# Kernel tuning notes

Measured on AMD Instinct MI355X. Metric: run time of the kernel, lower is better.

Reference implementation:

```python
import jax, jax.numpy as jnp
import numpy as np

B, S, D_IN, D_OUT, DEPTH = 4, 2048, 2048, 2048, 11
N_NODES = 2 ** (DEPTH + 1) - 1  # 4095


def setup_inputs() -> dict:
    key = jax.random.key(0)
    k1, k2, k3 = jax.random.split(key, 3)
    x = jax.random.normal(k1, (B, S, D_IN), dtype=jnp.float32)
    # scale weights like Linear init (~1/sqrt(fan_in)) to keep logits sane
    w_in = jax.random.normal(k2, (N_NODES, D_IN), dtype=jnp.float32) * (1.0 / np.sqrt(D_IN))
    w_out = jax.random.normal(k3, (D_OUT, N_NODES), dtype=jnp.float32) * (1.0 / np.sqrt(N_NODES))
    return {"x": x, "w_in": w_in, "w_out": w_out}


def reference(x, w_in, w_out):
    # x: [B,S,D_in]; w_in: [n_nodes, D_in]; w_out: [D_out, n_nodes]
    b, s, _ = x.shape
    cur = jnp.zeros((b, s), dtype=jnp.int32)
    nodes, logits = [], []
    for _ in range(DEPTH + 1):  # fixed, small depth loop (12 iters)
        nodes.append(cur)
        coeffs = w_in[cur]                       # [B,S,D_in] data-dependent gather
        score = jnp.einsum('bsd,bsd->bs', x, coeffs)  # per-token dot product
        logits.append(score)
        cur = cur * 2 + (score >= 0).astype(jnp.int32) + 1
    all_nodes = jnp.stack(nodes, axis=-1)        # [B,S,depth+1]
    all_logits = jnp.stack(logits, axis=-1)      # [B,S,depth+1]
    sel = w_out.T[all_nodes]                     # [B,S,depth+1,D_out]
    mlp1 = jax.nn.gelu(all_logits, approximate=False)  # torch nn.GELU default = exact erf
    return jnp.einsum('bsl,bslw->bsw', mlp1, sel)      # [B,S,D_out]
```

## Files before the change

kernel.cpp:

```cpp
#include <hip/hip_runtime.h>


#define D_IN    2048
#define D_OUT   2048
#define DEPTHP1 12
#define N_NODES 4095
#define N_TOK   8192
#define N_LEAF  2048

typedef float f4 __attribute__((ext_vector_type(4)));

__global__ __launch_bounds__(256) void transpose_wout64(
    const float* __restrict__ in, float* __restrict__ out) {
    __shared__ float tile[64][65];
    const int n0 = blockIdx.x * 64;
    const int j0 = blockIdx.y * 64;
    const int tx = threadIdx.x;
    const int ty = threadIdx.y;
    const int n = n0 + tx;
#pragma unroll
    for (int k = 0; k < 16; k++) {
        const int r = ty * 16 + k;
        if (n < N_NODES) tile[r][tx] = in[(size_t)(j0 + r) * N_NODES + n];
    }
    __syncthreads();
#pragma unroll
    for (int k = 0; k < 16; k++) {
        const int r = ty * 16 + k;
        const int nn = n0 + r;
        if (nn < N_NODES) out[(size_t)nn * D_OUT + (j0 + tx)] = tile[tx][r];
    }
}

__global__ __launch_bounds__(256) void phaseA(
    const float* __restrict__ x,
    const float* __restrict__ w_in,
    float* __restrict__ g_all,
    int* __restrict__ leaf,
    int* __restrict__ hist) {
    extern __shared__ float xs[];
    const int wave  = threadIdx.x >> 6;
    const int lane  = threadIdx.x & 63;
    const int token = blockIdx.x * 4 + wave;

    float4* xw = (float4*)(xs) + wave * (D_IN / 4);
    const float4* xrow = (const float4*)(x + (size_t)token * D_IN);
#pragma unroll
    for (int c = 0; c < 8; c++) xw[lane + 64 * c] = xrow[lane + 64 * c];

    int cur = 0;
#pragma unroll
    for (int l = 0; l < DEPTHP1; l++) {
        const float4* wrow = (const float4*)(w_in + (size_t)cur * D_IN);
        float p0 = 0.f, p1 = 0.f, p2 = 0.f, p3 = 0.f;
#pragma unroll
        for (int c = 0; c < 8; c++) {
            const float4 wc = wrow[lane + 64 * c];
            const float4 xc = xw[lane + 64 * c];
            float* p = (c < 2) ? &p0 : (c < 4) ? &p1 : (c < 6) ? &p2 : &p3;
            *p += wc.x * xc.x + wc.y * xc.y + wc.z * xc.z + wc.w * xc.w;
        }
        float part = (p0 + p1) + (p2 + p3);
#pragma unroll
        for (int off = 32; off >= 1; off >>= 1)
            part += __shfl_xor(part, off, 64);
        const float score = part;
        cur = 2 * cur + 1 + (score >= 0.f ? 1 : 0);
        const float g = 0.5f * score * (1.0f + erff(score * 0.70710678118654752f));
        if (lane == 0) g_all[token * DEPTHP1 + l] = g;
    }
    if (lane == 0) {
        const int leafid = ((cur - 1) >> 1) - (N_LEAF - 1);
        leaf[token] = leafid;
        atomicAdd(&hist[leafid], 1);
    }
}

__global__ __launch_bounds__(256) void init_counts(int* __restrict__ p) {
    const int i = blockIdx.x * 256 + threadIdx.x;
    if (i < 2 * N_LEAF) p[i] = 0;
}

__global__ __launch_bounds__(256) void scan2048(
    const int* __restrict__ hist, int* __restrict__ offsets ) {
    __shared__ int vals[N_LEAF];
    __shared__ int partial[256];
    const int t = threadIdx.x;
    int sum = 0;
#pragma unroll
    for (int k = 0; k < 8; k++) {
        const int v = hist[t * 8 + k];
        vals[t * 8 + k] = v;
        sum += v;
    }
    partial[t] = sum;
    __syncthreads();
    for (int off = 1; off < 256; off <<= 1) {
        const int v  = partial[t];
        const int vo = (t >= off) ? partial[t - off] : 0;
        __syncthreads();
        partial[t] = v + vo;
        __syncthreads();
    }
    int base = (t > 0) ? partial[t - 1] : 0;
#pragma unroll
    for (int k = 0; k < 8; k++) {
        offsets[t * 8 + k] = base;
        base += vals[t * 8 + k];
    }
    if (t == 255) offsets[N_LEAF] = base;
}

__global__ __launch_bounds__(256) void scatter_tokens(
    const int* __restrict__ leaf, const int* __restrict__ offsets,
    int* __restrict__ cnt, const float* __restrict__ g_all,
    int* __restrict__ order, float* __restrict__ g_sorted,
    int* __restrict__ lf_sorted) {
    const int t = blockIdx.x * 256 + threadIdx.x;
    if (t < N_TOK) {
        const int lf = leaf[t];
        const int pos = offsets[lf] + atomicAdd(&cnt[lf], 1);
        order[pos] = t;
        lf_sorted[pos] = lf;
#pragma unroll
        for (int l = 0; l < DEPTHP1; l++)
            g_sorted[(size_t)pos * DEPTHP1 + l] = g_all[(size_t)t * DEPTHP1 + l];
    }
}

__global__ __launch_bounds__(256) void phaseB_cols(
    const float* __restrict__ w_out_t,
    const float* __restrict__ g_sorted,
    const int* __restrict__ order,
    const int* __restrict__ lf_sorted,
    float* __restrict__ out) {
    const int b   = blockIdx.x;
    const int xcd = b & 7;
    const int j   = b >> 3;
    const int tr  = xcd * 32 + (j >> 1);
    const int ct  = j & 1;
    const int t   = threadIdx.x;
    const size_t coff = (size_t)ct * 1024 + (size_t)t * 4;

    const int start = tr * 32;
    const int end   = start + 32;

    int pos = start;
    while (pos < end) {
        const int lf = lf_sorted[pos];
        const int L  = lf + N_LEAF;
        f4 w[DEPTHP1];
#pragma unroll
        for (int l = 0; l < DEPTHP1; l++) {
            const int node = (L >> (DEPTHP1 - 1 - l)) - 1;
            w[l] = *(const f4*)(w_out_t + (size_t)node * D_OUT + coff);
        }
        do {
            const int tok = order[pos];
            const float* gp = g_sorted + (size_t)pos * DEPTHP1;
            f4 acc = {0.f, 0.f, 0.f, 0.f};
#pragma unroll
            for (int l = 0; l < DEPTHP1; l++)
                acc += gp[l] * w[l];
            *(f4*)(out + (size_t)tok * D_OUT + coff) = acc;
            pos++;
        } while (pos < end && lf_sorted[pos] == lf);
    }
}

template <bool TRANSPOSED>
__global__ __launch_bounds__(256) void fff_fused(
    const float* __restrict__ x, const float* __restrict__ w_in,
    const float* __restrict__ w_out, float* __restrict__ out) {
    const int wave  = threadIdx.x >> 6;
    const int lane  = threadIdx.x & 63;
    const int token = blockIdx.x * 4 + wave;
    const float4* xrow = (const float4*)(x + (size_t)token * D_IN);
    float xf[32];
#pragma unroll
    for (int c = 0; c < 8; c++) {
        float4 xc = xrow[lane + 64 * c];
        xf[c * 4 + 0] = xc.x; xf[c * 4 + 1] = xc.y;
        xf[c * 4 + 2] = xc.z; xf[c * 4 + 3] = xc.w;
    }
    float acc[32];
#pragma unroll
    for (int k = 0; k < 32; k++) acc[k] = 0.f;
    int cur = 0;
#pragma unroll
    for (int l = 0; l < DEPTHP1; l++) {
        const float4* wrow = (const float4*)(w_in + (size_t)cur * D_IN);
        float part = 0.f;
#pragma unroll
        for (int c = 0; c < 8; c++) {
            float4 wc = wrow[lane + 64 * c];
            part += wc.x * xf[c * 4 + 0]; part += wc.y * xf[c * 4 + 1];
            part += wc.z * xf[c * 4 + 2]; part += wc.w * xf[c * 4 + 3];
        }
#pragma unroll
        for (int off = 32; off >= 1; off >>= 1) part += __shfl_xor(part, off, 64);
        const float score = part;
        const float g = 0.5f * score * (1.0f + erff(score * 0.70710678118654752f));
        if (TRANSPOSED) {
            const float4* orow = (const float4*)(w_out + (size_t)cur * D_OUT);
#pragma unroll
            for (int c = 0; c < 8; c++) {
                float4 oc = orow[lane + 64 * c];
                acc[c * 4 + 0] += g * oc.x; acc[c * 4 + 1] += g * oc.y;
                acc[c * 4 + 2] += g * oc.z; acc[c * 4 + 3] += g * oc.w;
            }
        } else {
#pragma unroll
            for (int c = 0; c < 8; c++)
#pragma unroll
                for (int k = 0; k < 4; k++) {
                    const int j = (lane + 64 * c) * 4 + k;
                    acc[c * 4 + k] += g * w_out[(size_t)j * N_NODES + cur];
                }
        }
        cur = 2 * cur + 1 + (score >= 0.f ? 1 : 0);
    }
    float4* outrow = (float4*)(out + (size_t)token * D_OUT);
#pragma unroll
    for (int c = 0; c < 8; c++) {
        float4 o;
        o.x = acc[c * 4 + 0]; o.y = acc[c * 4 + 1];
        o.z = acc[c * 4 + 2]; o.w = acc[c * 4 + 3];
        outrow[lane + 64 * c] = o;
    }
}

extern "C" void kernel_launch(void* const* d_in, const int* in_sizes, int n_in,
                              void* d_out, int out_size, void* d_ws, size_t ws_size,
                              hipStream_t stream) {
    (void)in_sizes; (void)n_in; (void)out_size;
    const float* x     = (const float*)d_in[0];
    const float* w_in  = (const float*)d_in[1];
    const float* w_out = (const float*)d_in[2];
    float* out = (float*)d_out;

    const size_t wt_bytes   = (size_t)N_NODES * D_OUT * sizeof(float);
    const size_t g_bytes    = (size_t)N_TOK * DEPTHP1 * sizeof(float);
    const size_t leaf_bytes = (size_t)N_TOK * sizeof(int);
    const size_t ord_bytes  = (size_t)N_TOK * sizeof(int);
    const size_t hist_bytes = (size_t)N_LEAF * sizeof(int);
    const size_t cnt_bytes  = (size_t)N_LEAF * sizeof(int);
    const size_t offs_bytes = (size_t)(N_LEAF + 1) * sizeof(int);
    const size_t gs_bytes   = g_bytes;
    const size_t lfs_bytes  = (size_t)N_TOK * sizeof(int);
    const size_t need = wt_bytes + g_bytes + leaf_bytes + ord_bytes +
                        hist_bytes + cnt_bytes + offs_bytes + gs_bytes +
                        lfs_bytes + 64;

    if (ws_size >= need) {
        char* p = (char*)d_ws;
        float* w_out_t  = (float*)p;  p += wt_bytes;
        float* g_all    = (float*)p;  p += g_bytes;
        int*   leaf     = (int*)p;    p += leaf_bytes;
        int*   order    = (int*)p;    p += ord_bytes;
        int*   hist     = (int*)p;    p += hist_bytes;
        int*   cnt      = (int*)p;    p += cnt_bytes;
        int*   offsets  = (int*)p;    p += offs_bytes;
        float* g_sorted = (float*)p;  p += gs_bytes;
        int*   lf_sorted= (int*)p;

        init_counts<<<(2 * N_LEAF + 255) / 256, 256, 0, stream>>>(hist);
        transpose_wout64<<<dim3((N_NODES + 63) / 64, D_OUT / 64), dim3(64, 4),
                           0, stream>>>(w_out, w_out_t);
        phaseA<<<N_TOK / 4, 256, 4 * D_IN * sizeof(float), stream>>>(
            x, w_in, g_all, leaf, hist);
        scan2048<<<1, 256, 0, stream>>>(hist, offsets);
        scatter_tokens<<<N_TOK / 256, 256, 0, stream>>>(leaf, offsets, cnt,
                                                        g_all, order, g_sorted,
                                                        lf_sorted);
        phaseB_cols<<<512, 256, 0, stream>>>(w_out_t, g_sorted, order,
                                             lf_sorted, out);
    } else if (ws_size >= wt_bytes) {
        float* w_out_t = (float*)d_ws;
        transpose_wout64<<<dim3((N_NODES + 63) / 64, D_OUT / 64), dim3(64, 4),
                           0, stream>>>(w_out, w_out_t);
        fff_fused<true><<<N_TOK / 4, 256, 0, stream>>>(x, w_in, w_out_t, out);
    } else {
        fff_fused<false><<<N_TOK / 4, 256, 0, stream>>>(x, w_in, w_out, out);
    }
}
```

Baseline: 240.9 us.

## Use direct global-to-LDS loads in tree walk and finer phaseB grid with nontemporal stores

The tree-walk kernel becomes one wave per token and uses global_load_lds to stream the x row and each visited w_in row straight into LDS, waiting on vmcnt before each dot product. The output-combine kernel is launched with four times as many blocks, each covering 8 sorted tokens instead of 32, and writes the output with nontemporal stores. This aims to raise parallelism and memory throughput and to stop output writes from polluting the cache. In exchange, the tree walk serialises load and compute at every level, and smaller phaseB ranges reload the path weights more often.

Measured after the change: 240.9 us. No clear change (-0.0%).

```diff
diff --git a/kernel.cpp b/kernel.cpp
--- a/kernel.cpp
+++ b/kernel.cpp
@@ -9,6 +9,11 @@
 #define N_LEAF  2048
 
 typedef float f4 __attribute__((ext_vector_type(4)));
+
+#define GLDS16(gp, lp)                                                  \
+    __builtin_amdgcn_global_load_lds(                                   \
+        (const __attribute__((address_space(1))) void*)(gp),            \
+        (__attribute__((address_space(3))) void*)(lp), 16, 0, 0)
 
 __global__ __launch_bounds__(256) void transpose_wout64(
     const float* __restrict__ in, float* __restrict__ out) {
@@ -32,33 +37,42 @@
     }
 }
 
-__global__ __launch_bounds__(256) void phaseA(
+__global__ __launch_bounds__(64) void phaseA_gl(
     const float* __restrict__ x,
     const float* __restrict__ w_in,
     float* __restrict__ g_all,
     int* __restrict__ leaf,
     int* __restrict__ hist) {
-    extern __shared__ float xs[];
-    const int wave  = threadIdx.x >> 6;
-    const int lane  = threadIdx.x & 63;
-    const int token = blockIdx.x * 4 + wave;
-
-    float4* xw = (float4*)(xs) + wave * (D_IN / 4);
-    const float4* xrow = (const float4*)(x + (size_t)token * D_IN);
-#pragma unroll
-    for (int c = 0; c < 8; c++) xw[lane + 64 * c] = xrow[lane + 64 * c];
+    __shared__ float xs[D_IN];
+    __shared__ float wb[D_IN];
+    const int lane  = threadIdx.x;
+    const int token = blockIdx.x;
+
+    const float* xrow = x + (size_t)token * D_IN;
+#pragma unroll
+    for (int c = 0; c < 8; c++)
+        GLDS16(xrow + 4 * (lane + 64 * c), xs + c * 256);
+
+    const f4* xl = (const f4*)xs;
+    const f4* wl = (const f4*)wb;
 
     int cur = 0;
 #pragma unroll
     for (int l = 0; l < DEPTHP1; l++) {
-        const float4* wrow = (const float4*)(w_in + (size_t)cur * D_IN);
+        const float* wrow = w_in + (size_t)cur * D_IN;
+#pragma unroll
+        for (int c = 0; c < 8; c++)
+            GLDS16(wrow + 4 * (lane + 64 * c), wb + c * 256);
+        asm volatile("s_waitcnt vmcnt(0)" ::: "memory");
+        __builtin_amdgcn_sched_barrier(0);
+
         float p0 = 0.f, p1 = 0.f, p2 = 0.f, p3 = 0.f;
 #pragma unroll
         for (int c = 0; c < 8; c++) {
-            const float4 wc = wrow[lane + 64 * c];
-            const float4 xc = xw[lane + 64 * c];
+            const f4 wc = wl[lane + 64 * c];
+            const f4 xc = xl[lane + 64 * c];
             float* p = (c < 2) ? &p0 : (c < 4) ? &p1 : (c < 6) ? &p2 : &p3;
-            *p += wc.x * xc.x + wc.y * xc.y + wc.z * xc.z + wc.w * xc.w;
+            *p += wc[0] * xc[0] + wc[1] * xc[1] + wc[2] * xc[2] + wc[3] * xc[3];
         }
         float part = (p0 + p1) + (p2 + p3);
 #pragma unroll
@@ -137,13 +151,13 @@
     const int b   = blockIdx.x;
     const int xcd = b & 7;
     const int j   = b >> 3;
-    const int tr  = xcd * 32 + (j >> 1);
+    const int tr  = xcd * 128 + (j >> 1);
     const int ct  = j & 1;
     const int t   = threadIdx.x;
     const size_t coff = (size_t)ct * 1024 + (size_t)t * 4;
 
-    const int start = tr * 32;
-    const int end   = start + 32;
+    const int start = tr * 8;
+    const int end   = start + 8;
 
     int pos = start;
     while (pos < end) {
@@ -162,7 +176,8 @@
 #pragma unroll
             for (int l = 0; l < DEPTHP1; l++)
                 acc += gp[l] * w[l];
-            *(f4*)(out + (size_t)tok * D_OUT + coff) = acc;
+            __builtin_nontemporal_store(
+                acc, (f4*)(out + (size_t)tok * D_OUT + coff));
             pos++;
         } while (pos < end && lf_sorted[pos] == lf);
     }
@@ -267,14 +282,13 @@
         init_counts<<<(2 * N_LEAF + 255) / 256, 256, 0, stream>>>(hist);
         transpose_wout64<<<dim3((N_NODES + 63) / 64, D_OUT / 64), dim3(64, 4),
                            0, stream>>>(w_out, w_out_t);
-        phaseA<<<N_TOK / 4, 256, 4 * D_IN * sizeof(float), stream>>>(
-            x, w_in, g_all, leaf, hist);
+        phaseA_gl<<<N_TOK, 64, 0, stream>>>(x, w_in, g_all, leaf, hist);
         scan2048<<<1, 256, 0, stream>>>(hist, offsets);
         scatter_tokens<<<N_TOK / 256, 256, 0, stream>>>(leaf, offsets, cnt,
                                                         g_all, order, g_sorted,
                                                         lf_sorted);
-        phaseB_cols<<<512, 256, 0, stream>>>(w_out_t, g_sorted, order,
-                                             lf_sorted, out);
+        phaseB_cols<<<2048, 256, 0, stream>>>(w_out_t, g_sorted, order,
+                                              lf_sorted, out);
     } else if (ws_size >= wt_bytes) {
         float* w_out_t = (float*)d_ws;
         transpose_wout64<<<dim3((N_NODES + 63) / 64, D_OUT / 64), dim3(64, 4),
```

## Fuse counter init, scan and scatter; widen phaseB grid with nontemporal stores

Applied to the files above, without the earlier changes.

Zeroing of the histogram and counter arrays moves into the w_out transpose kernel. The single-block scan is merged into the scatter kernel, where every block recomputes the 2048-entry prefix sum in shared memory. Together these remove three kernel launches and the offsets buffer. phaseB_cols now runs 2048 blocks of 8 sorted tokens each instead of 512 blocks of 32, which raises parallelism but reloads leaf weights more often, and its output stores become nontemporal.

Measured after the change: 224.9 us. -6.7%, faster.

```diff
diff --git a/kernel.cpp b/kernel.cpp
--- a/kernel.cpp
+++ b/kernel.cpp
@@ -10,13 +10,19 @@
 
 typedef float f4 __attribute__((ext_vector_type(4)));
 
-__global__ __launch_bounds__(256) void transpose_wout64(
-    const float* __restrict__ in, float* __restrict__ out) {
+__global__ __launch_bounds__(256) void transpose_wout64z(
+    const float* __restrict__ in, float* __restrict__ out,
+    int* __restrict__ hc ) {
     __shared__ float tile[64][65];
+    const int fb = blockIdx.y * 64 + blockIdx.x;
+    const int tx = threadIdx.x;
+    const int ty = threadIdx.y;
+    if (fb < 16) {
+        const int i = fb * 256 + ty * 64 + tx;
+        hc[i] = 0;
+    }
     const int n0 = blockIdx.x * 64;
     const int j0 = blockIdx.y * 64;
-    const int tx = threadIdx.x;
-    const int ty = threadIdx.y;
     const int n = n0 + tx;
 #pragma unroll
     for (int k = 0; k < 16; k++) {
@@ -76,56 +82,46 @@
     }
 }
 
-__global__ __launch_bounds__(256) void init_counts(int* __restrict__ p) {
-    const int i = blockIdx.x * 256 + threadIdx.x;
-    if (i < 2 * N_LEAF) p[i] = 0;
-}
-
-__global__ __launch_bounds__(256) void scan2048(
-    const int* __restrict__ hist, int* __restrict__ offsets ) {
-    __shared__ int vals[N_LEAF];
-    __shared__ int partial[256];
-    const int t = threadIdx.x;
-    int sum = 0;
-#pragma unroll
-    for (int k = 0; k < 8; k++) {
-        const int v = hist[t * 8 + k];
-        vals[t * 8 + k] = v;
-        sum += v;
-    }
-    partial[t] = sum;
-    __syncthreads();
-    for (int off = 1; off < 256; off <<= 1) {
-        const int v  = partial[t];
-        const int vo = (t >= off) ? partial[t - off] : 0;
-        __syncthreads();
-        partial[t] = v + vo;
-        __syncthreads();
-    }
-    int base = (t > 0) ? partial[t - 1] : 0;
-#pragma unroll
-    for (int k = 0; k < 8; k++) {
-        offsets[t * 8 + k] = base;
-        base += vals[t * 8 + k];
-    }
-    if (t == 255) offsets[N_LEAF] = base;
-}
-
-__global__ __launch_bounds__(256) void scatter_tokens(
-    const int* __restrict__ leaf, const int* __restrict__ offsets,
+__global__ __launch_bounds__(256) void scatter_scan(
+    const int* __restrict__ leaf, const int* __restrict__ hist,
     int* __restrict__ cnt, const float* __restrict__ g_all,
     int* __restrict__ order, float* __restrict__ g_sorted,
     int* __restrict__ lf_sorted) {
-    const int t = blockIdx.x * 256 + threadIdx.x;
-    if (t < N_TOK) {
-        const int lf = leaf[t];
-        const int pos = offsets[lf] + atomicAdd(&cnt[lf], 1);
-        order[pos] = t;
-        lf_sorted[pos] = lf;
-#pragma unroll
-        for (int l = 0; l < DEPTHP1; l++)
-            g_sorted[(size_t)pos * DEPTHP1 + l] = g_all[(size_t)t * DEPTHP1 + l];
-    }
+    __shared__ int voff[N_LEAF];
+    __shared__ int partial[256];
+    const int t = threadIdx.x;
+    int v[8];
+    int sum = 0;
+#pragma unroll
+    for (int k = 0; k < 8; k++) {
+        v[k] = hist[t * 8 + k];
+        sum += v[k];
+    }
+    partial[t] = sum;
+    __syncthreads();
+    for (int off = 1; off < 256; off <<= 1) {
+        const int pv = partial[t];
+        const int po = (t >= off) ? partial[t - off] : 0;
+        __syncthreads();
+        partial[t] = pv + po;
+        __syncthreads();
+    }
+    int base = (t > 0) ? partial[t - 1] : 0;
+#pragma unroll
+    for (int k = 0; k < 8; k++) {
+        voff[t * 8 + k] = base;
+        base += v[k];
+    }
+    __syncthreads();
+
+    const int tok = blockIdx.x * 256 + t;
+    const int lf  = leaf[tok];
+    const int pos = voff[lf] + atomicAdd(&cnt[lf], 1);
+    order[pos] = tok;
+    lf_sorted[pos] = lf;
+#pragma unroll
+    for (int l = 0; l < DEPTHP1; l++)
+        g_sorted[(size_t)pos * DEPTHP1 + l] = g_all[(size_t)tok * DEPTHP1 + l];
 }
 
 __global__ __launch_bounds__(256) void phaseB_cols(
@@ -137,13 +133,13 @@
     const int b   = blockIdx.x;
     const int xcd = b & 7;
     const int j   = b >> 3;
-    const int tr  = xcd * 32 + (j >> 1);
+    const int tr  = xcd * 128 + (j >> 1);
     const int ct  = j & 1;
     const int t   = threadIdx.x;
     const size_t coff = (size_t)ct * 1024 + (size_t)t * 4;
 
-    const int start = tr * 32;
-    const int end   = start + 32;
+    const int start = tr * 8;
+    const int end   = start + 8;
 
     int pos = start;
     while (pos < end) {
@@ -162,9 +158,32 @@
 #pragma unroll
             for (int l = 0; l < DEPTHP1; l++)
                 acc += gp[l] * w[l];
-            *(f4*)(out + (size_t)tok * D_OUT + coff) = acc;
+            __builtin_nontemporal_store(
+                acc, (f4*)(out + (size_t)tok * D_OUT + coff));
             pos++;
         } while (pos < end && lf_sorted[pos] == lf);
+    }
+}
+
+__global__ __launch_bounds__(256) void transpose_wout64(
+    const float* __restrict__ in, float* __restrict__ out) {
+    __shared__ float tile[64][65];
+    const int n0 = blockIdx.x * 64;
+    const int j0 = blockIdx.y * 64;
+    const int tx = threadIdx.x;
+    const int ty = threadIdx.y;
+    const int n = n0 + tx;
+#pragma unroll
+    for (int k = 0; k < 16; k++) {
+        const int r = ty * 16 + k;
+        if (n < N_NODES) tile[r][tx] = in[(size_t)(j0 + r) * N_NODES + n];
+    }
+    __syncthreads();
+#pragma unroll
+    for (int k = 0; k < 16; k++) {
+        const int r = ty * 16 + k;
+        const int nn = n0 + r;
+        if (nn < N_NODES) out[(size_t)nn * D_OUT + (j0 + tx)] = tile[tx][r];
     }
 }
 
@@ -245,12 +264,10 @@
     const size_t ord_bytes  = (size_t)N_TOK * sizeof(int);
     const size_t hist_bytes = (size_t)N_LEAF * sizeof(int);
     const size_t cnt_bytes  = (size_t)N_LEAF * sizeof(int);
-    const size_t offs_bytes = (size_t)(N_LEAF + 1) * sizeof(int);
     const size_t gs_bytes   = g_bytes;
     const size_t lfs_bytes  = (size_t)N_TOK * sizeof(int);
     const size_t need = wt_bytes + g_bytes + leaf_bytes + ord_bytes +
-                        hist_bytes + cnt_bytes + offs_bytes + gs_bytes +
-                        lfs_bytes + 64;
+                        hist_bytes + cnt_bytes + gs_bytes + lfs_bytes + 64;
 
     if (ws_size >= need) {
         char* p = (char*)d_ws;
@@ -260,21 +277,17 @@
         int*   order    = (int*)p;    p += ord_bytes;
         int*   hist     = (int*)p;    p += hist_bytes;
         int*   cnt      = (int*)p;    p += cnt_bytes;
-        int*   offsets  = (int*)p;    p += offs_bytes;
         float* g_sorted = (float*)p;  p += gs_bytes;
         int*   lf_sorted= (int*)p;
 
-        init_counts<<<(2 * N_LEAF + 255) / 256, 256, 0, stream>>>(hist);
-        transpose_wout64<<<dim3((N_NODES + 63) / 64, D_OUT / 64), dim3(64, 4),
-                           0, stream>>>(w_out, w_out_t);
+        transpose_wout64z<<<dim3(64, 32), dim3(64, 4), 0, stream>>>(
+            w_out, w_out_t, hist);
         phaseA<<<N_TOK / 4, 256, 4 * D_IN * sizeof(float), stream>>>(
             x, w_in, g_all, leaf, hist);
-        scan2048<<<1, 256, 0, stream>>>(hist, offsets);
-        scatter_tokens<<<N_TOK / 256, 256, 0, stream>>>(leaf, offsets, cnt,
-                                                        g_all, order, g_sorted,
-                                                        lf_sorted);
-        phaseB_cols<<<512, 256, 0, stream>>>(w_out_t, g_sorted, order,
-                                             lf_sorted, out);
+        scatter_scan<<<N_TOK / 256, 256, 0, stream>>>(leaf, hist, cnt, g_all,
+                                                      order, g_sorted, lf_sorted);
+        phaseB_cols<<<2048, 256, 0, stream>>>(w_out_t, g_sorted, order,
+                                              lf_sorted, out);
     } else if (ws_size >= wt_bytes) {
         float* w_out_t = (float*)d_ws;
         transpose_wout64<<<dim3((N_NODES + 63) / 64, D_OUT / 64), dim3(64, 4),
```
